# Kernel optimization log

Measured on AMD Instinct MI355X. Metric: run time of the kernel, lower is better.

Reference implementation:

```python
import jax, jax.numpy as jnp
import numpy as np

D = 3  # interpolation dimensionality (trilinear)


def nd_corners(d):
    # corner offsets of the d-dim unit hypercube: [1, 2^d, d] int32
    xi = [jnp.arange(2, dtype=jnp.int32) for _ in range(d)]
    return jnp.stack(jnp.meshgrid(*xi, indexing='ij'), -1).reshape(1, 2 ** d, d)


def setup_inputs() -> dict:
    key = jax.random.key(0)
    k1, k2 = jax.random.split(key)
    input = jax.random.normal(k1, (16, 128, 128, 128), dtype=jnp.float32)
    # normalized coords in [-1, 1]
    coords = jax.random.uniform(k2, (1000000, 3), dtype=jnp.float32) * 2.0 - 1.0
    return {"input": input, "coords": coords}


def reference(input, coords):
    d = D
    grid_shape = jnp.asarray(input.shape[-d:], dtype=coords.dtype)  # [d]
    # _unnormalize: map [-1, 1] -> grid coords
    c = (coords + 1.0) / 2.0 * (grid_shape - 1.0)
    S = c.shape[:-1]
    c = c.reshape(-1, 1, d)                      # [N, 1, d]
    corners = nd_corners(d)                       # [1, 2^d, d]
    floor = jnp.floor(c)
    # weights_fn: |x - floor(x) + i - 1|, product over dims -> [N, 2^d]
    weights = jnp.abs(c - floor + corners.astype(c.dtype) - 1.0).prod(-1)
    # index_fn + nearest clamp
    index = floor.astype(jnp.int32) + corners     # [N, 2^d, d]
    high = jnp.asarray(input.shape[-d:], dtype=jnp.int32)
    index = jnp.clip(index, 0, high - 1)
    # gather corner values: input[..., i0, i1, i2] -> [C, N, 2^d]
    values = input[..., index[..., 0], index[..., 1], index[..., 2]]
    out = (weights * values).sum(-1)              # [C, N]
    return out.reshape(*input.shape[:-d], *S)
```

## Files before the change

kernel.cpp:

```cpp
#include <hip/hip_runtime.h>
#include <hip/hip_bf16.h>


#define GD   128
#define NCH  16
constexpr int VOX = GD * GD * GD;

__global__ __launch_bounds__(256) void transpose_k(const float* __restrict__ in,
                                                   float* __restrict__ ws) {
    int s = blockIdx.x * 256 + threadIdx.x;
    float v[NCH];
#pragma unroll
    for (int c = 0; c < NCH; ++c)
        v[c] = in[(size_t)c * VOX + s];
    float4* o = (float4*)(ws + (size_t)s * NCH);
    o[0] = make_float4(v[0],  v[1],  v[2],  v[3]);
    o[1] = make_float4(v[4],  v[5],  v[6],  v[7]);
    o[2] = make_float4(v[8],  v[9],  v[10], v[11]);
    o[3] = make_float4(v[12], v[13], v[14], v[15]);
}

__device__ __forceinline__ void fma4(float4& a, float w, const float4 v) {
    a.x += w * v.x; a.y += w * v.y; a.z += w * v.z; a.w += w * v.w;
}

__global__ __launch_bounds__(256) void interp_k(const float* __restrict__ ws,
                                                const float* __restrict__ coords,
                                                float* __restrict__ out, int N) {
    int n = blockIdx.x * 256 + threadIdx.x;
    if (n >= N) return;

    float cx = (coords[3 * n + 0] + 1.0f) * 0.5f * (float)(GD - 1);
    float cy = (coords[3 * n + 1] + 1.0f) * 0.5f * (float)(GD - 1);
    float cz = (coords[3 * n + 2] + 1.0f) * 0.5f * (float)(GD - 1);

    float fx = floorf(cx), fy = floorf(cy), fz = floorf(cz);
    float tx = cx - fx, ty = cy - fy, tz = cz - fz;
    int ix = (int)fx, iy = (int)fy, iz = (int)fz;

    int ix0 = min(max(ix,     0), GD - 1), ix1 = min(max(ix + 1, 0), GD - 1);
    int iy0 = min(max(iy,     0), GD - 1), iy1 = min(max(iy + 1, 0), GD - 1);
    int iz0 = min(max(iz,     0), GD - 1), iz1 = min(max(iz + 1, 0), GD - 1);

    float wx0 = 1.0f - tx, wx1 = tx;
    float wy0 = 1.0f - ty, wy1 = ty;
    float wz0 = 1.0f - tz, wz1 = tz;

    size_t bx0 = (size_t)ix0 * (GD * GD * NCH), bx1 = (size_t)ix1 * (GD * GD * NCH);
    size_t by0 = (size_t)iy0 * (GD * NCH),      by1 = (size_t)iy1 * (GD * NCH);
    size_t bz0 = (size_t)iz0 * NCH,             bz1 = (size_t)iz1 * NCH;

    float4 a0 = {0,0,0,0}, a1 = {0,0,0,0}, a2 = {0,0,0,0}, a3 = {0,0,0,0};

#define CORNER(BX, BY, BZ, W)                                        \
    {                                                                \
        const float4* p = (const float4*)(ws + (BX) + (BY) + (BZ));  \
        float w = (W);                                               \
        fma4(a0, w, p[0]); fma4(a1, w, p[1]);                        \
        fma4(a2, w, p[2]); fma4(a3, w, p[3]);                        \
    }

    CORNER(bx0, by0, bz0, wx0 * wy0 * wz0)
    CORNER(bx0, by0, bz1, wx0 * wy0 * wz1)
    CORNER(bx0, by1, bz0, wx0 * wy1 * wz0)
    CORNER(bx0, by1, bz1, wx0 * wy1 * wz1)
    CORNER(bx1, by0, bz0, wx1 * wy0 * wz0)
    CORNER(bx1, by0, bz1, wx1 * wy0 * wz1)
    CORNER(bx1, by1, bz0, wx1 * wy1 * wz0)
    CORNER(bx1, by1, bz1, wx1 * wy1 * wz1)
#undef CORNER

    out[(size_t)0  * N + n] = a0.x; out[(size_t)1  * N + n] = a0.y;
    out[(size_t)2  * N + n] = a0.z; out[(size_t)3  * N + n] = a0.w;
    out[(size_t)4  * N + n] = a1.x; out[(size_t)5  * N + n] = a1.y;
    out[(size_t)6  * N + n] = a1.z; out[(size_t)7  * N + n] = a1.w;
    out[(size_t)8  * N + n] = a2.x; out[(size_t)9  * N + n] = a2.y;
    out[(size_t)10 * N + n] = a2.z; out[(size_t)11 * N + n] = a2.w;
    out[(size_t)12 * N + n] = a3.x; out[(size_t)13 * N + n] = a3.y;
    out[(size_t)14 * N + n] = a3.z; out[(size_t)15 * N + n] = a3.w;
}

__global__ __launch_bounds__(256) void interp_direct_k(const float* __restrict__ in,
                                                       const float* __restrict__ coords,
                                                       float* __restrict__ out, int N) {
    int n = blockIdx.x * 256 + threadIdx.x;
    if (n >= N) return;

    float cx = (coords[3 * n + 0] + 1.0f) * 0.5f * (float)(GD - 1);
    float cy = (coords[3 * n + 1] + 1.0f) * 0.5f * (float)(GD - 1);
    float cz = (coords[3 * n + 2] + 1.0f) * 0.5f * (float)(GD - 1);

    float fx = floorf(cx), fy = floorf(cy), fz = floorf(cz);
    float tx = cx - fx, ty = cy - fy, tz = cz - fz;
    int ix = (int)fx, iy = (int)fy, iz = (int)fz;

    int ix0 = min(max(ix,     0), GD - 1), ix1 = min(max(ix + 1, 0), GD - 1);
    int iy0 = min(max(iy,     0), GD - 1), iy1 = min(max(iy + 1, 0), GD - 1);
    int iz0 = min(max(iz,     0), GD - 1), iz1 = min(max(iz + 1, 0), GD - 1);

    float wx0 = 1.0f - tx, wx1 = tx;
    float wy0 = 1.0f - ty, wy1 = ty;
    float wz0 = 1.0f - tz, wz1 = tz;

    int o000 = (ix0 * GD + iy0) * GD + iz0, o001 = (ix0 * GD + iy0) * GD + iz1;
    int o010 = (ix0 * GD + iy1) * GD + iz0, o011 = (ix0 * GD + iy1) * GD + iz1;
    int o100 = (ix1 * GD + iy0) * GD + iz0, o101 = (ix1 * GD + iy0) * GD + iz1;
    int o110 = (ix1 * GD + iy1) * GD + iz0, o111 = (ix1 * GD + iy1) * GD + iz1;

    float w000 = wx0 * wy0 * wz0, w001 = wx0 * wy0 * wz1;
    float w010 = wx0 * wy1 * wz0, w011 = wx0 * wy1 * wz1;
    float w100 = wx1 * wy0 * wz0, w101 = wx1 * wy0 * wz1;
    float w110 = wx1 * wy1 * wz0, w111 = wx1 * wy1 * wz1;

#pragma unroll
    for (int c = 0; c < NCH; ++c) {
        const float* g = in + (size_t)c * VOX;
        float acc = w000 * g[o000] + w001 * g[o001] + w010 * g[o010] + w011 * g[o011]
                  + w100 * g[o100] + w101 * g[o101] + w110 * g[o110] + w111 * g[o111];
        out[(size_t)c * N + n] = acc;
    }
}

extern "C" void kernel_launch(void* const* d_in, const int* in_sizes, int n_in,
                              void* d_out, int out_size, void* d_ws, size_t ws_size,
                              hipStream_t stream) {
    const float* input  = (const float*)d_in[0];
    const float* coords = (const float*)d_in[1];
    float* out = (float*)d_out;
    int N = in_sizes[1] / 3;

    size_t need = (size_t)VOX * NCH * sizeof(float);
    if (ws_size >= need) {
        transpose_k<<<VOX / 256, 256, 0, stream>>>(input, (float*)d_ws);
        interp_k<<<(N + 255) / 256, 256, 0, stream>>>((const float*)d_ws, coords, out, N);
    } else {
        interp_direct_k<<<(N + 255) / 256, 256, 0, stream>>>(input, coords, out, N);
    }
}
```

Before: 374.1 us.

## Store transposed channel-last volume as bf16 to halve gather traffic

The transpose kernel now packs the channel-last copy of the volume into bf16 with round-to-nearest-even. It also reads float4 from each channel plane, so each thread handles four voxels. The interpolation kernel gathers 32-byte bf16 corner records instead of 64-byte fp32 ones and expands them to fp32 for accumulation, which halves transpose writes and gather bytes. The cost is bf16 precision loss in the sampled values, which may exceed the accuracy tolerance.

```diff
diff --git a/kernel.cpp b/kernel.cpp
--- a/kernel.cpp
+++ b/kernel.cpp
@@ -6,27 +6,40 @@
 #define NCH  16
 constexpr int VOX = GD * GD * GD;
 
-__global__ __launch_bounds__(256) void transpose_k(const float* __restrict__ in,
-                                                   float* __restrict__ ws) {
-    int s = blockIdx.x * 256 + threadIdx.x;
-    float v[NCH];
+__device__ __forceinline__ unsigned short f2bf_rne(float f) {
+    unsigned u = __builtin_bit_cast(unsigned, f);
+    u = u + 0x7fffu + ((u >> 16) & 1u);
+    return (unsigned short)(u >> 16);
+}
+
+__global__ __launch_bounds__(256) void transpose_bf16_k(const float* __restrict__ in,
+                                                        unsigned short* __restrict__ ws) {
+    int t = blockIdx.x * 256 + threadIdx.x;
+    int s = t * 4;
+    float4 v[NCH];
 #pragma unroll
     for (int c = 0; c < NCH; ++c)
-        v[c] = in[(size_t)c * VOX + s];
-    float4* o = (float4*)(ws + (size_t)s * NCH);
-    o[0] = make_float4(v[0],  v[1],  v[2],  v[3]);
-    o[1] = make_float4(v[4],  v[5],  v[6],  v[7]);
-    o[2] = make_float4(v[8],  v[9],  v[10], v[11]);
-    o[3] = make_float4(v[12], v[13], v[14], v[15]);
+        v[c] = *(const float4*)(in + (size_t)c * VOX + s);
+
+    const float* vf = (const float*)v;
+#pragma unroll
+    for (int j = 0; j < 4; ++j) {
+        unsigned p[8];
+#pragma unroll
+        for (int k = 0; k < 8; ++k) {
+            unsigned lo = f2bf_rne(vf[(2 * k + 0) * 4 + j]);
+            unsigned hi = f2bf_rne(vf[(2 * k + 1) * 4 + j]);
+            p[k] = lo | (hi << 16);
+        }
+        uint4* o = (uint4*)(ws + (size_t)(s + j) * NCH);
+        o[0] = make_uint4(p[0], p[1], p[2], p[3]);
+        o[1] = make_uint4(p[4], p[5], p[6], p[7]);
+    }
 }
 
-__device__ __forceinline__ void fma4(float4& a, float w, const float4 v) {
-    a.x += w * v.x; a.y += w * v.y; a.z += w * v.z; a.w += w * v.w;
-}
-
-__global__ __launch_bounds__(256) void interp_k(const float* __restrict__ ws,
-                                                const float* __restrict__ coords,
-                                                float* __restrict__ out, int N) {
+__global__ __launch_bounds__(256) void interp_bf16_k(const unsigned short* __restrict__ ws,
+                                                     const float* __restrict__ coords,
+                                                     float* __restrict__ out, int N) {
     int n = blockIdx.x * 256 + threadIdx.x;
     if (n >= N) return;
 
@@ -50,14 +63,23 @@
     size_t by0 = (size_t)iy0 * (GD * NCH),      by1 = (size_t)iy1 * (GD * NCH);
     size_t bz0 = (size_t)iz0 * NCH,             bz1 = (size_t)iz1 * NCH;
 
-    float4 a0 = {0,0,0,0}, a1 = {0,0,0,0}, a2 = {0,0,0,0}, a3 = {0,0,0,0};
+    float acc[NCH];
+#pragma unroll
+    for (int c = 0; c < NCH; ++c) acc[c] = 0.0f;
 
-#define CORNER(BX, BY, BZ, W)                                        \
-    {                                                                \
-        const float4* p = (const float4*)(ws + (BX) + (BY) + (BZ));  \
-        float w = (W);                                               \
-        fma4(a0, w, p[0]); fma4(a1, w, p[1]);                        \
-        fma4(a2, w, p[2]); fma4(a3, w, p[3]);                        \
+#define CORNER(BX, BY, BZ, W)                                                  \
+    {                                                                          \
+        const uint4* p = (const uint4*)(ws + (BX) + (BY) + (BZ));              \
+        uint4 A = p[0], B = p[1];                                              \
+        unsigned u[8] = {A.x, A.y, A.z, A.w, B.x, B.y, B.z, B.w};              \
+        float w = (W);                                                         \
+        _Pragma("unroll")                                                      \
+        for (int k = 0; k < 8; ++k) {                                          \
+            float lo = __builtin_bit_cast(float, u[k] << 16);                  \
+            float hi = __builtin_bit_cast(float, u[k] & 0xffff0000u);          \
+            acc[2 * k + 0] += w * lo;                                          \
+            acc[2 * k + 1] += w * hi;                                          \
+        }                                                                      \
     }
 
     CORNER(bx0, by0, bz0, wx0 * wy0 * wz0)
@@ -70,14 +92,9 @@
     CORNER(bx1, by1, bz1, wx1 * wy1 * wz1)
 #undef CORNER
 
-    out[(size_t)0  * N + n] = a0.x; out[(size_t)1  * N + n] = a0.y;
-    out[(size_t)2  * N + n] = a0.z; out[(size_t)3  * N + n] = a0.w;
-    out[(size_t)4  * N + n] = a1.x; out[(size_t)5  * N + n] = a1.y;
-    out[(size_t)6  * N + n] = a1.z; out[(size_t)7  * N + n] = a1.w;
-    out[(size_t)8  * N + n] = a2.x; out[(size_t)9  * N + n] = a2.y;
-    out[(size_t)10 * N + n] = a2.z; out[(size_t)11 * N + n] = a2.w;
-    out[(size_t)12 * N + n] = a3.x; out[(size_t)13 * N + n] = a3.y;
-    out[(size_t)14 * N + n] = a3.z; out[(size_t)15 * N + n] = a3.w;
+#pragma unroll
+    for (int c = 0; c < NCH; ++c)
+        out[(size_t)c * N + n] = acc[c];
 }
 
 __global__ __launch_bounds__(256) void interp_direct_k(const float* __restrict__ in,
@@ -129,10 +146,11 @@
     float* out = (float*)d_out;
     int N = in_sizes[1] / 3;
 
-    size_t need = (size_t)VOX * NCH * sizeof(float);
+    size_t need = (size_t)VOX * NCH * sizeof(unsigned short);
     if (ws_size >= need) {
-        transpose_k<<<VOX / 256, 256, 0, stream>>>(input, (float*)d_ws);
-        interp_k<<<(N + 255) / 256, 256, 0, stream>>>((const float*)d_ws, coords, out, N);
+        transpose_bf16_k<<<VOX / 4 / 256, 256, 0, stream>>>(input, (unsigned short*)d_ws);
+        interp_bf16_k<<<(N + 255) / 256, 256, 0, stream>>>((const unsigned short*)d_ws,
+                                                           coords, out, N);
     } else {
         interp_direct_k<<<(N + 255) / 256, 256, 0, stream>>>(input, coords, out, N);
     }
```

Measured after the change: 355.7 us. -4.9%, faster.
